# Optimization experiments

Measured on AMD Instinct MI355X. Metric: run time of the kernel, lower is better.

The kernel has to match this reference:

```python
import jax, jax.numpy as jnp
import numpy as np

B, S, D = 2, 1024, 1024
H, HD = 16, 64          # n_heads, head_dim (H*HD == D)
E, FF = 8, 2816         # num_experts, moe hidden_dim
TOP_K = 2               # hard-coded torch.topk(scores, 2)
EPS = 1e-5


def rmsnorm(x, w):
    return x * jax.lax.rsqrt(jnp.mean(x * x, axis=-1, keepdims=True) + EPS) * w


def apply_rope(x, cos, sin):
    # x: [B,S,H,HD]; cos/sin: [S,HD//2] -> interleaved rotary (llama style)
    xr, xi = x[..., 0::2], x[..., 1::2]
    c = cos[None, :, None, :]
    s = sin[None, :, None, :]
    out_r = xr * c - xi * s
    out_i = xr * s + xi * c
    return jnp.stack([out_r, out_i], axis=-1).reshape(x.shape)


def setup_inputs() -> dict:
    key = jax.random.key(0)
    ks = jax.random.split(key, 10)
    sc = 0.02
    pos = jnp.arange(S, dtype=jnp.float32)
    inv = 1.0 / (10000.0 ** (jnp.arange(0, HD, 2, dtype=jnp.float32) / HD))
    ang = pos[:, None] * inv[None, :]                       # [S, HD//2]
    return {
        "x": jax.random.normal(ks[0], (B, S, D), jnp.float32),
        "freqs_cos": jnp.cos(ang),
        "freqs_sin": jnp.sin(ang),
        "attn_norm_w": jnp.ones((D,), jnp.float32),
        "wq": jax.random.normal(ks[1], (D, D), jnp.float32) * sc,
        "wk": jax.random.normal(ks[2], (D, D), jnp.float32) * sc,
        "wv": jax.random.normal(ks[3], (D, D), jnp.float32) * sc,
        "wo": jax.random.normal(ks[4], (D, D), jnp.float32) * sc,
        "ffn_norm_w": jnp.ones((D,), jnp.float32),
        "gate_w": jax.random.normal(ks[5], (E, D), jnp.float32) * sc,
        "w1": jax.random.normal(ks[6], (E, FF, D), jnp.float32) * sc,
        "w2": jax.random.normal(ks[7], (E, FF, D), jnp.float32) * sc,
        "w3": jax.random.normal(ks[8], (E, FF, D), jnp.float32) * sc,
    }


def reference(x, freqs_cos, freqs_sin, attn_norm_w, wq, wk, wv, wo,
              ffn_norm_w, gate_w, w1, w2, w3):
    b, s, d = x.shape

    # ---- pre-norm attention + residual ----
    xn = rmsnorm(x, attn_norm_w)
    q = (xn @ wq.T).reshape(b, s, H, HD)
    k = (xn @ wk.T).reshape(b, s, H, HD)
    v = (xn @ wv.T).reshape(b, s, H, HD)
    q = apply_rope(q, freqs_cos, freqs_sin)
    k = apply_rope(k, freqs_cos, freqs_sin)
    scores = jnp.einsum("bqhd,bkhd->bhqk", q, k) / jnp.sqrt(jnp.float32(HD))
    causal = jnp.tril(jnp.ones((s, s), bool))
    scores = jnp.where(causal[None, None], scores, jnp.finfo(scores.dtype).min)
    attn = jax.nn.softmax(scores, axis=-1)
    o = jnp.einsum("bhqk,bkhd->bqhd", attn, v).reshape(b, s, d) @ wo.T
    h = x + o

    # ---- top-2 MoE FFN (math identical to gather-per-token einsums) ----
    t = rmsnorm(h, ffn_norm_w).reshape(-1, d)               # [T, D]
    T = t.shape[0]
    gate = t @ gate_w.T                                     # [T, E]
    expert_weights, expert_idx = jax.lax.top_k(gate, TOP_K)
    expert_weights = jax.nn.softmax(expert_weights, axis=-1)  # [T, 2]

    x1 = jax.nn.silu(jnp.einsum("td,efd->tef", t, w1))      # [T, E, FF]
    x3 = jnp.einsum("td,efd->tef", t, w3)                   # [T, E, FF]
    ta = jnp.arange(T)[:, None]
    g = x1[ta, expert_idx] * x3[ta, expert_idx]             # [T, 2, FF]
    gw = g * expert_weights[..., None]                      # fold routing weights
    h_full = jnp.zeros((T, E, FF), t.dtype).at[ta, expert_idx].add(gw)
    moe = jnp.einsum("tef,efd->td", h_full, w2)             # [T, D]

    return h + moe.reshape(b, s, d)
```

## Files before the change

kernel.cpp:

```cpp
#include <hip/hip_runtime.h>

#define DI __device__ __forceinline__

typedef __attribute__((ext_vector_type(8))) short short8;
typedef __attribute__((ext_vector_type(4))) float f32x4;

#define DM   1024
#define TT   2048
#define SEQ  1024
#define NHD  16
#define HDD  64
#define NE   8
#define FF   2816

DI ushort f2bf(float f){
  union { float f; unsigned u; } c; c.f = f;
  unsigned u = c.u;
  u += 0x7fffu + ((u >> 16) & 1u);
  return (ushort)(u >> 16);
}
DI float bf2f(ushort b){
  union { unsigned u; float f; } c; c.u = ((unsigned)b) << 16;
  return c.f;
}
DI unsigned pk2(float a, float b){ return (unsigned)f2bf(a) | ((unsigned)f2bf(b) << 16); }
DI uint2 mku2(unsigned a, unsigned b){ uint2 r; r.x = a; r.y = b; return r; }

DI f32x4 MFMA(short8 a, short8 b, f32x4 c){
  return __builtin_amdgcn_mfma_f32_16x16x32_bf16(a, b, c, 0, 0, 0);
}

DI void gload16(const void* g, void* l){
  __builtin_amdgcn_global_load_lds(
      (const __attribute__((address_space(1))) unsigned*)g,
      (__attribute__((address_space(3))) unsigned*)l, 16, 0, 0);
}

#define LDSWZB(row, p) (((row) * 128) + ((((p) ^ ((row) & 7))) * 16))

__global__ __launch_bounds__(256) void k_rmsnorm(const float* __restrict__ x,
                                                 const float* __restrict__ w,
                                                 ushort* __restrict__ xh,
                                                 ushort* __restrict__ xl)
{
  int row = blockIdx.x, tid = threadIdx.x;
  float4 v = ((const float4*)(x + (size_t)row * DM))[tid];
  float ss = v.x*v.x + v.y*v.y + v.z*v.z + v.w*v.w;
#pragma unroll
  for (int m = 32; m >= 1; m >>= 1) ss += __shfl_xor(ss, m);
  __shared__ float sh[4];
  if ((tid & 63) == 0) sh[tid >> 6] = ss;
  __syncthreads();
  ss = sh[0] + sh[1] + sh[2] + sh[3];
  float rstd = 1.0f / sqrtf(ss * (1.0f / DM) + 1e-5f);
  float4 wv = ((const float4*)w)[tid];
  float o0 = v.x * rstd * wv.x, o1 = v.y * rstd * wv.y;
  float o2 = v.z * rstd * wv.z, o3 = v.w * rstd * wv.w;
  ushort h0 = f2bf(o0), h1 = f2bf(o1), h2 = f2bf(o2), h3 = f2bf(o3);
  ((uint2*)(xh + (size_t)row * DM))[tid] =
      mku2((unsigned)h0 | ((unsigned)h1 << 16), (unsigned)h2 | ((unsigned)h3 << 16));
  ((uint2*)(xl + (size_t)row * DM))[tid] =
      mku2(pk2(o0 - bf2f(h0), o1 - bf2f(h1)), pk2(o2 - bf2f(h2), o3 - bf2f(h3)));
}

__global__ __launch_bounds__(256) void k_wsplit(
    const float* __restrict__ wq, const float* __restrict__ wk,
    const float* __restrict__ wv, const float* __restrict__ wo,
    ushort* __restrict__ qh, ushort* __restrict__ ql,
    ushort* __restrict__ kh, ushort* __restrict__ kl,
    ushort* __restrict__ vh, ushort* __restrict__ vl,
    ushort* __restrict__ oh, ushort* __restrict__ ol)
{
  int y = blockIdx.y;
  const float* W = y == 0 ? wq : (y == 1 ? wk : (y == 2 ? wv : wo));
  ushort* H = y == 0 ? qh : (y == 1 ? kh : (y == 2 ? vh : oh));
  ushort* L = y == 0 ? ql : (y == 1 ? kl : (y == 2 ? vl : ol));
  int i = blockIdx.x * 256 + threadIdx.x;
  float4 v = ((const float4*)W)[i];
  ushort h0 = f2bf(v.x), h1 = f2bf(v.y), h2 = f2bf(v.z), h3 = f2bf(v.w);
  ((uint2*)H)[i] = mku2((unsigned)h0 | ((unsigned)h1 << 16),
                        (unsigned)h2 | ((unsigned)h3 << 16));
  ((uint2*)L)[i] = mku2(pk2(v.x - bf2f(h0), v.y - bf2f(h1)),
                        pk2(v.z - bf2f(h2), v.w - bf2f(h3)));
}

__global__ __launch_bounds__(256) void k_cw13(const float* __restrict__ w1,
                                              const float* __restrict__ w3,
                                              ushort* __restrict__ w1b,
                                              ushort* __restrict__ w3b)
{
  const float* src = blockIdx.y ? w3 : w1;
  ushort* dst = blockIdx.y ? w3b : w1b;
  const size_t N4 = (size_t)NE * FF * DM / 4;
  for (size_t i = (size_t)blockIdx.x * 256 + threadIdx.x; i < N4;
       i += (size_t)gridDim.x * 256) {
    float4 v = ((const float4*)src)[i];
    ((uint2*)dst)[i] = mku2(pk2(v.x, v.y), pk2(v.z, v.w));
  }
}

__global__ __launch_bounds__(256) void k_tw2(const float* __restrict__ w2, ushort* __restrict__ w2t)
{
  int dt = blockIdx.x, ft = blockIdx.y, e = blockIdx.z;
  __shared__ ushort lt[64*72];
  int tid = threadIdx.x;
#pragma unroll
  for (int i = 0; i < 4; i++) {
    int c = tid + i*256;
    int r = c >> 4, q = c & 15;
    float4 v = *(const float4*)(w2 + ((size_t)e*FF + ft*64 + r) * DM + dt*64 + q*4);
    lt[(q*4+0)*72 + r] = f2bf(v.x);
    lt[(q*4+1)*72 + r] = f2bf(v.y);
    lt[(q*4+2)*72 + r] = f2bf(v.z);
    lt[(q*4+3)*72 + r] = f2bf(v.w);
  }
  __syncthreads();
#pragma unroll
  for (int i = 0; i < 2; i++) {
    int c = tid + i*256;
    int d = c >> 3, fq = c & 7;
    *(uint4*)(w2t + ((size_t)e*DM + dt*64 + d) * FF + ft*64 + fq*8) = *(const uint4*)&lt[d*72 + fq*8];
  }
}

__global__ __launch_bounds__(256, 2) void k_gemm_qkv(
    const ushort* __restrict__ xh, const ushort* __restrict__ xl,
    const ushort* __restrict__ wqh, const ushort* __restrict__ wql,
    const ushort* __restrict__ wkh, const ushort* __restrict__ wkl,
    const ushort* __restrict__ wvh, const ushort* __restrict__ wvl,
    const float* __restrict__ fc, const float* __restrict__ fs,
    ushort* __restrict__ qh, ushort* __restrict__ ql,
    ushort* __restrict__ kh, ushort* __restrict__ kl,
    ushort* __restrict__ vh, ushort* __restrict__ vl)
{
  __shared__ __align__(16) char lds[65536];
  char* Ah = lds;          char* Al = lds + 16384;
  char* Bh = lds + 32768;  char* Bl = lds + 49152;
  int bn = blockIdx.x, bm = blockIdx.y;
  int which = bn >> 3, bnn = bn & 7;
  const ushort* WH = which == 0 ? wqh : (which == 1 ? wkh : wvh);
  const ushort* WL = which == 0 ? wql : (which == 1 ? wkl : wvl);
  int tid = threadIdx.x, lane = tid & 63, w = tid >> 6, wr = w >> 1, wc = w & 1;
  int r0 = lane >> 3, pp = lane & 7;
  size_t asrc[4], bsrc[4]; int cdst[4];
#pragma unroll
  for (int i = 0; i < 4; i++) {
    int c = w * 4 + i;
    int row = c * 8 + r0;
    asrc[i] = (size_t)(bm * 128 + row) * DM + (pp ^ r0) * 8;
    bsrc[i] = (size_t)(bnn * 128 + row) * DM + (pp ^ r0) * 8;
    cdst[i] = c * 1024;
  }
  f32x4 acc[4][4] = {};
  for (int kb = 0; kb < DM; kb += 64) {
    __syncthreads();
#pragma unroll
    for (int i = 0; i < 4; i++) {
      gload16(xh + asrc[i] + kb, Ah + cdst[i]);
      gload16(xl + asrc[i] + kb, Al + cdst[i]);
      gload16(WH + bsrc[i] + kb, Bh + cdst[i]);
      gload16(WL + bsrc[i] + kb, Bl + cdst[i]);
    }
    __syncthreads();
#pragma unroll
    for (int kk = 0; kk < 2; kk++) {
      int j = kk * 4 + (lane >> 4);
      short8 ar[4], al[4];
#pragma unroll
      for (int mi = 0; mi < 4; mi++) {
        int row = wr * 64 + mi * 16 + (lane & 15);
        ar[mi] = *(const short8*)(Ah + LDSWZB(row, j));
        al[mi] = *(const short8*)(Al + LDSWZB(row, j));
      }
#pragma unroll
      for (int ni = 0; ni < 4; ni++) {
        int n = wc * 64 + ni * 16 + (lane & 15);
        short8 b_h = *(const short8*)(Bh + LDSWZB(n, j));
        short8 b_l = *(const short8*)(Bl + LDSWZB(n, j));
#pragma unroll
        for (int mi = 0; mi < 4; mi++) {
          acc[mi][ni] = MFMA(ar[mi], b_h, acc[mi][ni]);
          acc[mi][ni] = MFMA(al[mi], b_h, acc[mi][ni]);
          acc[mi][ni] = MFMA(ar[mi], b_l, acc[mi][ni]);
        }
      }
    }
  }
  ushort* OH = which == 0 ? qh : kh;
  ushort* OL = which == 0 ? ql : kl;
#pragma unroll
  for (int mi = 0; mi < 4; mi++)
#pragma unroll
    for (int ni = 0; ni < 4; ni++)
#pragma unroll
      for (int r = 0; r < 4; r++) {
        int rg = bm*128 + wr*64 + mi*16 + (lane >> 4)*4 + r;
        int cg = bnn*128 + wc*64 + ni*16 + (lane & 15);
        float v = acc[mi][ni][r];
        int b = rg >> 10, s = rg & 1023, hh = cg >> 6, hd = cg & 63;
        if (which <= 1) {
          float p = __shfl_xor(v, 1);
          int pi = hd >> 1;
          float c = fc[s*32 + pi], sn = fs[s*32 + pi];
          float rr = (hd & 1) ? (p * sn + v * c) : (v * c - p * sn);
          size_t o = ((size_t)(b*NHD + hh) * SEQ + s) * HDD + hd;
          ushort hv = f2bf(rr);
          OH[o] = hv; OL[o] = f2bf(rr - bf2f(hv));
        } else {
          size_t o = ((size_t)((b*NHD + hh)*HDD + hd)) * SEQ + s;
          ushort hv = f2bf(v);
          vh[o] = hv; vl[o] = f2bf(v - bf2f(hv));
        }
      }
}

__global__ __launch_bounds__(256) void k_attn_prep(
    const ushort* __restrict__ qh_, const ushort* __restrict__ ql_,
    const ushort* __restrict__ kh_, const ushort* __restrict__ kl_,
    const ushort* __restrict__ vh_, const ushort* __restrict__ vl_,
    ushort* __restrict__ oh_, ushort* __restrict__ ol_,
    const float* __restrict__ w1, const float* __restrict__ w3,
    ushort* __restrict__ w1b, ushort* __restrict__ w3b,
    const float* __restrict__ w2, ushort* __restrict__ w2t)
{
  __shared__ __align__(16) char smem[49152];
  int bid = blockIdx.x, tid = threadIdx.x;

  if (bid >= 1024) {
    ushort* lt = (ushort*)smem;
    int pid = bid - 1024;
    for (int tt = pid; tt < 16*44*8; tt += 512) {
      int dt = tt & 15, rest = tt >> 4;
      int ft = rest % 44, e = rest / 44;
#pragma unroll
      for (int i = 0; i < 4; i++) {
        int c = tid + i*256;
        int r = c >> 4, q = c & 15;
        float4 v = *(const float4*)(w2 + ((size_t)e*FF + ft*64 + r) * DM + dt*64 + q*4);
        lt[(q*4+0)*72 + r] = f2bf(v.x);
        lt[(q*4+1)*72 + r] = f2bf(v.y);
        lt[(q*4+2)*72 + r] = f2bf(v.z);
        lt[(q*4+3)*72 + r] = f2bf(v.w);
      }
      __syncthreads();
#pragma unroll
      for (int i = 0; i < 2; i++) {
        int c = tid + i*256;
        int d = c >> 3, fq = c & 7;
        *(uint4*)(w2t + ((size_t)e*DM + dt*64 + d) * FF + ft*64 + fq*8) =
            *(const uint4*)&lt[d*72 + fq*8];
      }
      __syncthreads();
    }
    return;
  }
  if (bid >= 512) {
    int pid = bid - 512;
    const size_t N4 = (size_t)NE * FF * DM / 4;
    for (size_t i = (size_t)pid * 256 + tid; i < N4; i += (size_t)512 * 256) {
      float4 v = ((const float4*)w1)[i];
      ((uint2*)w1b)[i] = mku2(pk2(v.x, v.y), pk2(v.z, v.w));
      float4 u = ((const float4*)w3)[i];
      ((uint2*)w3b)[i] = mku2(pk2(u.x, u.y), pk2(u.z, u.w));
    }
    return;
  }

  char* Kh = smem;          char* Kl = smem + 8192;
  char* Vh = smem + 16384;  char* Vl = smem + 24576;
  ushort* Ph = (ushort*)(smem + 32768);
  ushort* Pl = (ushort*)(smem + 40960);
  int qt = bid & 15, bh = bid >> 4;
  int lane = tid & 63, w = tid >> 6;
  int r0 = lane >> 3, pp = lane & 7;
  short8 qfh[2], qfl[2];
  int qrow = qt*64 + w*16 + (lane & 15);
#pragma unroll
  for (int ks = 0; ks < 2; ks++) {
    size_t g = ((size_t)bh * SEQ + qrow) * HDD + ks*32 + (lane >> 4)*8;
    qfh[ks] = *(const short8*)(qh_ + g);
    qfl[ks] = *(const short8*)(ql_ + g);
  }
  size_t kbase[2], vbase[2];
#pragma unroll
  for (int i = 0; i < 2; i++) {
    int c = 2*w + i;
    kbase[i] = ((size_t)bh * SEQ + c*8 + r0) * 64 + (pp ^ r0) * 8;
    vbase[i] = ((size_t)bh * 64 + c*8 + r0) * SEQ + (pp ^ r0) * 8;
  }
  f32x4 oacc[4] = {};
  float mrun[4], lrun[4];
#pragma unroll
  for (int r = 0; r < 4; r++) { mrun[r] = -1e30f; lrun[r] = 0.0f; }

  for (int kt = 0; kt <= qt; kt++) {
    __syncthreads();
#pragma unroll
    for (int i = 0; i < 2; i++) {
      int c = 2*w + i;
      size_t ko = kbase[i] + (size_t)kt * 64 * 64;
      size_t vo = vbase[i] + (size_t)kt * 64;
      gload16(kh_ + ko, Kh + c*1024);
      gload16(kl_ + ko, Kl + c*1024);
      gload16(vh_ + vo, Vh + c*1024);
      gload16(vl_ + vo, Vl + c*1024);
    }
    __syncthreads();
    f32x4 sa[4] = {};
#pragma unroll
    for (int j2 = 0; j2 < 4; j2++) {
#pragma unroll
      for (int ks = 0; ks < 2; ks++) {
        int kr = j2*16 + (lane & 15);
        int j = ks*4 + (lane >> 4);
        short8 b_h = *(const short8*)(Kh + LDSWZB(kr, j));
        short8 b_l = *(const short8*)(Kl + LDSWZB(kr, j));
        sa[j2] = MFMA(qfh[ks], b_h, sa[j2]);
        sa[j2] = MFMA(qfl[ks], b_h, sa[j2]);
        sa[j2] = MFMA(qfh[ks], b_l, sa[j2]);
      }
    }
    float sv[4][4];
#pragma unroll
    for (int j2 = 0; j2 < 4; j2++)
#pragma unroll
      for (int r = 0; r < 4; r++) {
        float xx = sa[j2][r] * 0.125f;
        if (kt == qt) {
          int kv = j2*16 + (lane & 15), qi = w*16 + (lane >> 4)*4 + r;
          if (kv > qi) xx = -1e30f;
        }
        sv[j2][r] = xx;
      }
#pragma unroll
    for (int r = 0; r < 4; r++) {
      float mx = fmaxf(fmaxf(sv[0][r], sv[1][r]), fmaxf(sv[2][r], sv[3][r]));
#pragma unroll
      for (int m = 8; m >= 1; m >>= 1) mx = fmaxf(mx, __shfl_xor(mx, m));
      float mn = fmaxf(mrun[r], mx);
      float alp = __expf(mrun[r] - mn);
      mrun[r] = mn;
      float rs = 0.0f;
#pragma unroll
      for (int j2 = 0; j2 < 4; j2++) { float pv = __expf(sv[j2][r] - mn); sv[j2][r] = pv; rs += pv; }
#pragma unroll
      for (int m = 8; m >= 1; m >>= 1) rs += __shfl_xor(rs, m);
      lrun[r] = lrun[r] * alp + rs;
#pragma unroll
      for (int hf = 0; hf < 4; hf++) oacc[hf][r] *= alp;
    }
#pragma unroll
    for (int j2 = 0; j2 < 4; j2++)
#pragma unroll
      for (int r = 0; r < 4; r++) {
        int row = (lane >> 4)*4 + r, col = j2*16 + (lane & 15);
        int d = w*1024 + row*64 + (((col >> 3) ^ (row & 7)) * 8) + (col & 7);
        ushort hv = f2bf(sv[j2][r]);
        Ph[d] = hv; Pl[d] = f2bf(sv[j2][r] - bf2f(hv));
      }
#pragma unroll
    for (int hf = 0; hf < 4; hf++) {
#pragma unroll
      for (int ks = 0; ks < 2; ks++) {
        int prow = lane & 15;
        int j = ks*4 + (lane >> 4);
        int pg = (j ^ (prow & 7)) * 8;
        short8 pfh = *(const short8*)&Ph[w*1024 + prow*64 + pg];
        short8 pfl = *(const short8*)&Pl[w*1024 + prow*64 + pg];
        int vrow = hf*16 + (lane & 15);
        short8 vfh = *(const short8*)(Vh + LDSWZB(vrow, j));
        short8 vfl = *(const short8*)(Vl + LDSWZB(vrow, j));
        oacc[hf] = MFMA(pfh, vfh, oacc[hf]);
        oacc[hf] = MFMA(pfl, vfh, oacc[hf]);
        oacc[hf] = MFMA(pfh, vfl, oacc[hf]);
      }
    }
  }
  int b = bh >> 4, h = bh & 15;
#pragma unroll
  for (int r = 0; r < 4; r++) {
    float li = 1.0f / lrun[r];
    int srow = qt*64 + w*16 + (lane >> 4)*4 + r;
#pragma unroll
    for (int hf = 0; hf < 4; hf++) {
      float v = oacc[hf][r] * li;
      size_t o = ((size_t)(b*SEQ + srow)) * DM + h*HDD + hf*16 + (lane & 15);
      ushort hv = f2bf(v);
      oh_[o] = hv; ol_[o] = f2bf(v - bf2f(hv));
    }
  }
}

__global__ __launch_bounds__(256, 3) void k_gemm_wo(
    const ushort* __restrict__ oh, const ushort* __restrict__ ol,
    const ushort* __restrict__ woh, const ushort* __restrict__ wol,
    const float* __restrict__ x, float* __restrict__ hb)
{
  __shared__ __align__(16) char lds[49152];
  char* Ah = lds;          char* Al = lds + 8192;
  char* Bh = lds + 16384;  char* Bl = lds + 32768;
  int bnn = blockIdx.x, bm = blockIdx.y;
  int tid = threadIdx.x, lane = tid & 63, w = tid >> 6;
  int r0 = lane >> 3, pp = lane & 7;
  size_t asrc[2]; int adst[2];
#pragma unroll
  for (int i = 0; i < 2; i++) {
    int c = w * 2 + i;
    int row = c * 8 + r0;
    asrc[i] = (size_t)(bm * 64 + row) * DM + (pp ^ r0) * 8;
    adst[i] = c * 1024;
  }
  size_t bsrc[4]; int bdst[4];
#pragma unroll
  for (int i = 0; i < 4; i++) {
    int c = w * 4 + i;
    int row = c * 8 + r0;
    bsrc[i] = (size_t)(bnn * 128 + row) * DM + (pp ^ r0) * 8;
    bdst[i] = c * 1024;
  }
  f32x4 acc[4][2] = {};
  for (int kb = 0; kb < DM; kb += 64) {
    __syncthreads();
#pragma unroll
    for (int i = 0; i < 2; i++) {
      gload16(oh + asrc[i] + kb, Ah + adst[i]);
      gload16(ol + asrc[i] + kb, Al + adst[i]);
    }
#pragma unroll
    for (int i = 0; i < 4; i++) {
      gload16(woh + bsrc[i] + kb, Bh + bdst[i]);
      gload16(wol + bsrc[i] + kb, Bl + bdst[i]);
    }
    __syncthreads();
#pragma unroll
    for (int kk = 0; kk < 2; kk++) {
      int j = kk * 4 + (lane >> 4);
      short8 ar[4], al[4];
#pragma unroll
      for (int mi = 0; mi < 4; mi++) {
        int row = mi * 16 + (lane & 15);
        ar[mi] = *(const short8*)(Ah + LDSWZB(row, j));
        al[mi] = *(const short8*)(Al + LDSWZB(row, j));
      }
#pragma unroll
      for (int ni = 0; ni < 2; ni++) {
        int n = w * 32 + ni * 16 + (lane & 15);
        short8 b_h = *(const short8*)(Bh + LDSWZB(n, j));
        short8 b_l = *(const short8*)(Bl + LDSWZB(n, j));
#pragma unroll
        for (int mi = 0; mi < 4; mi++) {
          acc[mi][ni] = MFMA(ar[mi], b_h, acc[mi][ni]);
          acc[mi][ni] = MFMA(al[mi], b_h, acc[mi][ni]);
          acc[mi][ni] = MFMA(ar[mi], b_l, acc[mi][ni]);
        }
      }
    }
  }
#pragma unroll
  for (int mi = 0; mi < 4; mi++)
#pragma unroll
    for (int ni = 0; ni < 2; ni++)
#pragma unroll
      for (int r = 0; r < 4; r++) {
        int rg = bm*64 + mi*16 + (lane >> 4)*4 + r;
        int cg = bnn*128 + w*32 + ni*16 + (lane & 15);
        hb[(size_t)rg * DM + cg] = x[(size_t)rg * DM + cg] + acc[mi][ni][r];
      }
}

__global__ __launch_bounds__(256) void k_gate(
    const float* __restrict__ hb, const float* __restrict__ fw, const float* __restrict__ gwt,
    ushort* __restrict__ tb, int* __restrict__ idx, float* __restrict__ ew, int* __restrict__ cnt)
{
  int t = blockIdx.x, tid = threadIdx.x;
  float4 v = ((const float4*)(hb + (size_t)t * DM))[tid];
  float ss = v.x*v.x + v.y*v.y + v.z*v.z + v.w*v.w;
#pragma unroll
  for (int m = 32; m >= 1; m >>= 1) ss += __shfl_xor(ss, m);
  __shared__ float sh[4];
  if ((tid & 63) == 0) sh[tid >> 6] = ss;
  __syncthreads();
  ss = sh[0] + sh[1] + sh[2] + sh[3];
  float rstd = 1.0f / sqrtf(ss * (1.0f / DM) + 1e-5f);
  float4 wv = ((const float4*)fw)[tid];
  float tv0 = v.x*rstd*wv.x, tv1 = v.y*rstd*wv.y, tv2 = v.z*rstd*wv.z, tv3 = v.w*rstd*wv.w;
  ((uint2*)(tb + (size_t)t * DM))[tid] = mku2(pk2(tv0, tv1), pk2(tv2, tv3));
  float ge[8];
#pragma unroll
  for (int e = 0; e < 8; e++) {
    float4 gv = ((const float4*)(gwt + (size_t)e * DM))[tid];
    float s = tv0*gv.x + tv1*gv.y + tv2*gv.z + tv3*gv.w;
#pragma unroll
    for (int m = 32; m >= 1; m >>= 1) s += __shfl_xor(s, m);
    ge[e] = s;
  }
  __shared__ float gsh[4][8];
  if ((tid & 63) == 0) {
#pragma unroll
    for (int e = 0; e < 8; e++) gsh[tid >> 6][e] = ge[e];
  }
  __syncthreads();
  if (tid == 0) {
    float lg[8];
#pragma unroll
    for (int e = 0; e < 8; e++) lg[e] = gsh[0][e] + gsh[1][e] + gsh[2][e] + gsh[3][e];
    int i0 = 0;
    for (int e = 1; e < 8; e++) if (lg[e] > lg[i0]) i0 = e;
    int i1 = (i0 == 0) ? 1 : 0;
    for (int e = 0; e < 8; e++) if (e != i0 && lg[e] > lg[i1]) i1 = e;
    float ex = __expf(lg[i1] - lg[i0]);
    idx[2*t] = i0; idx[2*t+1] = i1;
    ew[2*t] = 1.0f / (1.0f + ex); ew[2*t+1] = ex / (1.0f + ex);
    atomicAdd(&cnt[i0], 1); atomicAdd(&cnt[i1], 1);
  }
}

__global__ void k_offsets(const int* __restrict__ cnt, int* __restrict__ off,
                          int* __restrict__ fil, int* __restrict__ tmap)
{
  if (threadIdx.x == 0 && blockIdx.x == 0) {
    int a = 0, nt = 0;
    for (int e = 0; e < 8; e++) {
      off[e] = a; a += cnt[e]; fil[e] = 0;
      int m = (cnt[e] + 127) >> 7;
      for (int j = 0; j < m; j++) { tmap[1 + nt] = (e << 8) | j; nt++; }
    }
    tmap[0] = nt;
  }
}

__global__ __launch_bounds__(256) void k_scatter(
    const int* __restrict__ idx, const int* __restrict__ off,
    int* __restrict__ fil, int* __restrict__ ent, int* __restrict__ pos)
{
  int t = blockIdx.x * 256 + threadIdx.x;
  if (t < TT) {
#pragma unroll
    for (int k = 0; k < 2; k++) {
      int e = idx[2*t + k];
      int p = atomicAdd(&fil[e], 1);
      int g = off[e] + p;
      ent[g] = 2*t + k;
      pos[2*t + k] = g;
    }
  }
}

__global__ __launch_bounds__(256, 4) void k_moe13(
    const ushort* __restrict__ tb, const ushort* __restrict__ w1b, const ushort* __restrict__ w3b,
    const int* __restrict__ ent, const float* __restrict__ ew,
    const int* __restrict__ cnt, const int* __restrict__ off, const int* __restrict__ tmap,
    ushort* __restrict__ gb)
{
  int y = blockIdx.y;
  if (y >= tmap[0]) return;
  int tm = tmap[1 + y];
  int e = tm >> 8, mt = tm & 255;
  int nt = blockIdx.x;
  int cn = cnt[e], oe = off[e];
  __shared__ __align__(16) char lds[32768];
  char* Ab = lds;
  char* B1 = lds + 16384;
  char* B3 = lds + 24576;
  int tid = threadIdx.x, lane = tid & 63, w = tid >> 6;
  int wr = w >> 1, wc = w & 1;
  int r0 = lane >> 3, pp = lane & 7;

  const ushort* abase = tb + (pp ^ r0) * 8;
  unsigned aoff[4];
#pragma unroll
  for (int i = 0; i < 4; i++) {
    int c = w * 4 + i;
    int r = c * 8 + r0;
    int g = oe + mt * 128 + r; if (g > 2*TT - 1) g = 2*TT - 1;
    aoff[i] = (unsigned)((ent[g] >> 1) * DM);
  }
  size_t bofs[2];
#pragma unroll
  for (int i = 0; i < 2; i++) {
    int c = 2 * w + i;
    bofs[i] = ((size_t)e * FF + nt * 64 + c * 8 + r0) * DM + (pp ^ r0) * 8;
  }

  f32x4 acc1[4][2] = {}, acc3[4][2] = {};

  for (int kb = 0; kb < DM; kb += 64) {
    __syncthreads();
#pragma unroll
    for (int i = 0; i < 4; i++)
      gload16(abase + aoff[i] + kb, Ab + (w * 4 + i) * 1024);
#pragma unroll
    for (int i = 0; i < 2; i++) {
      gload16(w1b + bofs[i] + kb, B1 + (2 * w + i) * 1024);
      gload16(w3b + bofs[i] + kb, B3 + (2 * w + i) * 1024);
    }
    __syncthreads();
#pragma unroll
    for (int kk = 0; kk < 2; kk++) {
      int j = kk * 4 + (lane >> 4);
      short8 af[4];
#pragma unroll
      for (int mi = 0; mi < 4; mi++) {
        int row = wr * 64 + mi * 16 + (lane & 15);
        af[mi] = *(const short8*)(Ab + LDSWZB(row, j));
      }
#pragma unroll
      for (int ni = 0; ni < 2; ni++) {
        int n = wc * 32 + ni * 16 + (lane & 15);
        short8 b1f = *(const short8*)(B1 + LDSWZB(n, j));
        short8 b3f = *(const short8*)(B3 + LDSWZB(n, j));
#pragma unroll
        for (int mi = 0; mi < 4; mi++) {
          acc1[mi][ni] = MFMA(af[mi], b1f, acc1[mi][ni]);
          acc3[mi][ni] = MFMA(af[mi], b3f, acc3[mi][ni]);
        }
      }
    }
  }
#pragma unroll
  for (int mi = 0; mi < 4; mi++)
#pragma unroll
    for (int ni = 0; ni < 2; ni++)
#pragma unroll
      for (int r = 0; r < 4; r++) {
        int grow = mt * 128 + wr * 64 + mi * 16 + (lane >> 4) * 4 + r;
        if (grow < cn) {
          int g = oe + grow;
          float gwv = ew[ent[g]];
          int f = nt * 64 + wc * 32 + ni * 16 + (lane & 15);
          float x1 = acc1[mi][ni][r], x3 = acc3[mi][ni][r];
          float sg = x1 / (1.0f + __expf(-x1));
          gb[(size_t)g * FF + f] = f2bf(sg * x3 * gwv);
        }
      }
}

__global__ __launch_bounds__(256, 4) void k_moe2(
    const ushort* __restrict__ gb, const ushort* __restrict__ w2t,
    const int* __restrict__ cnt, const int* __restrict__ off, const int* __restrict__ tmap,
    float* __restrict__ mr)
{
  int y = blockIdx.y;
  if (y >= tmap[0]) return;
  int tm = tmap[1 + y];
  int e = tm >> 8, mt = tm & 255;
  int nt = blockIdx.x;
  int cn = cnt[e], oe = off[e];
  __shared__ __align__(16) char lds[24576];
  char* Ab = lds; char* Bb = lds + 16384;
  int tid = threadIdx.x, lane = tid & 63, w = tid >> 6;
  int r0 = lane >> 3, pp = lane & 7;

  const ushort* abase = gb + (pp ^ r0) * 8;
  unsigned aoff[4];
#pragma unroll
  for (int i = 0; i < 4; i++) {
    int c = w * 4 + i;
    int r = c * 8 + r0;
    int g = oe + mt * 128 + r; if (g > 2*TT - 1) g = 2*TT - 1;
    aoff[i] = (unsigned)(g * FF);
  }
  size_t bofs[2];
#pragma unroll
  for (int i = 0; i < 2; i++) {
    int c = 2 * w + i;
    bofs[i] = ((size_t)e * DM + nt * 64 + c * 8 + r0) * FF + (pp ^ r0) * 8;
  }

  f32x4 a2[2][4] = {};
  for (int kb = 0; kb < FF; kb += 64) {
    __syncthreads();
#pragma unroll
    for (int i = 0; i < 4; i++)
      gload16(abase + aoff[i] + kb, Ab + (w * 4 + i) * 1024);
#pragma unroll
    for (int i = 0; i < 2; i++)
      gload16(w2t + bofs[i] + kb, Bb + (2 * w + i) * 1024);
    __syncthreads();
#pragma unroll
    for (int kk = 0; kk < 2; kk++) {
      int j = kk * 4 + (lane >> 4);
      short8 af[2], bf[4];
#pragma unroll
      for (int mi = 0; mi < 2; mi++) {
        int row = w * 32 + mi * 16 + (lane & 15);
        af[mi] = *(const short8*)(Ab + LDSWZB(row, j));
      }
#pragma unroll
      for (int ni = 0; ni < 4; ni++) {
        int n = ni * 16 + (lane & 15);
        bf[ni] = *(const short8*)(Bb + LDSWZB(n, j));
      }
#pragma unroll
      for (int ni = 0; ni < 4; ni++)
#pragma unroll
        for (int mi = 0; mi < 2; mi++)
          a2[mi][ni] = MFMA(af[mi], bf[ni], a2[mi][ni]);
    }
  }
#pragma unroll
  for (int mi = 0; mi < 2; mi++)
#pragma unroll
    for (int ni = 0; ni < 4; ni++)
#pragma unroll
      for (int r = 0; r < 4; r++) {
        int grow = mt * 128 + w * 32 + mi * 16 + (lane >> 4) * 4 + r;
        if (grow < cn) {
          int cg = nt * 64 + ni * 16 + (lane & 15);
          mr[(size_t)(oe + grow) * DM + cg] = a2[mi][ni][r];
        }
      }
}

__global__ __launch_bounds__(256) void k_final(
    const float* __restrict__ hb, const float* __restrict__ mr,
    const int* __restrict__ pos, float* __restrict__ out)
{
  int t = blockIdx.x, tid = threadIdx.x;
  int g0 = pos[2*t], g1 = pos[2*t+1];
  float4 a  = ((const float4*)(hb + (size_t)t * DM))[tid];
  float4 m0 = ((const float4*)(mr + (size_t)g0 * DM))[tid];
  float4 m1 = ((const float4*)(mr + (size_t)g1 * DM))[tid];
  float4 o;
  o.x = a.x + m0.x + m1.x; o.y = a.y + m0.y + m1.y;
  o.z = a.z + m0.z + m1.z; o.w = a.w + m0.w + m1.w;
  ((float4*)(out + (size_t)t * DM))[tid] = o;
}

extern "C" void kernel_launch(void* const* d_in, const int* in_sizes, int n_in,
                              void* d_out, int out_size, void* d_ws, size_t ws_size,
                              hipStream_t stream)
{
  const float* x   = (const float*)d_in[0];
  const float* fc  = (const float*)d_in[1];
  const float* fs  = (const float*)d_in[2];
  const float* anw = (const float*)d_in[3];
  const float* wq  = (const float*)d_in[4];
  const float* wk  = (const float*)d_in[5];
  const float* wv  = (const float*)d_in[6];
  const float* wo  = (const float*)d_in[7];
  const float* fnw = (const float*)d_in[8];
  const float* gwm = (const float*)d_in[9];
  const float* w1  = (const float*)d_in[10];
  const float* w2  = (const float*)d_in[11];
  const float* w3  = (const float*)d_in[12];
  float* out = (float*)d_out;

  char* p = (char*)d_ws;
  auto alloc = [&](size_t n) { char* r = p; p += (n + 255) & ~(size_t)255; return r; };
  ushort* xnh = (ushort*)alloc((size_t)TT*DM*2);
  ushort* xnl = (ushort*)alloc((size_t)TT*DM*2);
  char*   pad = alloc((size_t)8*1024*1024);
  ushort* qh  = (ushort*)alloc((size_t)TT*DM*2);
  ushort* ql  = (ushort*)alloc((size_t)TT*DM*2);
  ushort* kh  = (ushort*)alloc((size_t)TT*DM*2);
  ushort* kl  = (ushort*)alloc((size_t)TT*DM*2);
  ushort* vh  = (ushort*)alloc((size_t)TT*DM*2);
  ushort* vl  = (ushort*)alloc((size_t)TT*DM*2);
  ushort* oh  = (ushort*)alloc((size_t)TT*DM*2);
  ushort* ol  = (ushort*)alloc((size_t)TT*DM*2);
  float*  hb  = (float*) alloc((size_t)TT*DM*4);
  ushort* tb  = (ushort*)alloc((size_t)TT*DM*2);
  ushort* w2t = (ushort*)alloc((size_t)NE*FF*DM*2);
  ushort* gb  = (ushort*)alloc((size_t)2*TT*FF*2);
  float*  mr  = (float*) alloc((size_t)2*TT*DM*4);
  int*    idx = (int*)   alloc((size_t)2*TT*4);
  float*  ew  = (float*) alloc((size_t)2*TT*4);
  int*    ent = (int*)   alloc((size_t)2*TT*4);
  int*    pos = (int*)   alloc((size_t)2*TT*4);
  int*    cnt = (int*)   alloc(32);
  int*    off = (int*)   alloc(32);
  int*    fil = (int*)   alloc(32);
  int*    tmap= (int*)   alloc(256);
  (void)pad;

  ushort* wsp = (ushort*)mr;
  const size_t WN = (size_t)DM * DM;
  ushort* wqh = wsp;        ushort* wql = wsp + WN;
  ushort* wkh = wsp + 2*WN; ushort* wkl = wsp + 3*WN;
  ushort* wvh = wsp + 4*WN; ushort* wvl = wsp + 5*WN;
  ushort* woh = wsp + 6*WN; ushort* wol = wsp + 7*WN;

  ushort* w3b = (ushort*)alloc((size_t)NE*FF*DM*2);
  ushort* w1b_fresh = (ushort*)alloc((size_t)NE*FF*DM*2);
  bool big = ((size_t)(p - (char*)d_ws) <= ws_size);
  ushort* w1b = big ? w1b_fresh : (ushort*)d_ws;

  hipMemsetAsync(cnt, 0, 32, stream);
  k_rmsnorm<<<TT, 256, 0, stream>>>(x, anw, xnh, xnl);
  k_wsplit<<<dim3(1024, 4), 256, 0, stream>>>(wq, wk, wv, wo,
      wqh, wql, wkh, wkl, wvh, wvl, woh, wol);
  k_gemm_qkv<<<dim3(24, 16), 256, 0, stream>>>(xnh, xnl,
      wqh, wql, wkh, wkl, wvh, wvl, fc, fs, qh, ql, kh, kl, vh, vl);
  if (big) {
    k_attn_prep<<<1536, 256, 0, stream>>>(qh, ql, kh, kl, vh, vl, oh, ol,
        w1, w3, w1b, w3b, w2, w2t);
  } else {
    k_tw2<<<dim3(16, 44, 8), 256, 0, stream>>>(w2, w2t);
    k_attn_prep<<<512, 256, 0, stream>>>(qh, ql, kh, kl, vh, vl, oh, ol,
        w1, w3, w1b, w3b, w2, w2t);
  }
  k_gemm_wo<<<dim3(8, 32), 256, 0, stream>>>(oh, ol, woh, wol, x, hb);
  k_gate<<<TT, 256, 0, stream>>>(hb, fnw, gwm, tb, idx, ew, cnt);
  k_offsets<<<1, 64, 0, stream>>>(cnt, off, fil, tmap);
  k_scatter<<<8, 256, 0, stream>>>(idx, off, fil, ent, pos);
  if (!big) {
    k_cw13<<<dim3(2048, 2), 256, 0, stream>>>(w1, w3, w1b, w3b);
  }
  k_moe13<<<dim3(44, 48), 256, 0, stream>>>(tb, w1b, w3b, ent, ew, cnt, off, tmap, gb);
  k_moe2<<<dim3(16, 48), 256, 0, stream>>>(gb, w2t, cnt, off, tmap, mr);
  k_final<<<TT, 256, 0, stream>>>(hb, mr, pos, out);
  (void)in_sizes; (void)n_in; (void)out_size;
}
```

Baseline: 418.8 us.

## Merge prep kernels and overlap w2 transpose with QKV GEMM

Fuses the rmsnorm and attention-weight split into one launch, and moves the w2 transpose/bf16 conversion from the attention-prep kernel into extra blocks of the QKV GEMM launch, so that memory-bound transpose work runs alongside the compute-bound GEMM. The gate kernel now records per-expert slot positions from its atomic counters, and a single-block kernel computes the offsets and scatters entries, replacing two launches and the second atomic pass. This cuts launch count and rebalances work across kernels. The cost is possible contention between GEMM and transpose blocks, and a serial single-block offset/scatter kernel.

Result: faster. 393.9 us (-5.9%).

```diff
diff --git a/kernel.cpp b/kernel.cpp
--- a/kernel.cpp
+++ b/kernel.cpp
@@ -38,12 +38,33 @@
 
 #define LDSWZB(row, p) (((row) * 128) + ((((p) ^ ((row) & 7))) * 16))
 
-__global__ __launch_bounds__(256) void k_rmsnorm(const float* __restrict__ x,
-                                                 const float* __restrict__ w,
-                                                 ushort* __restrict__ xh,
-                                                 ushort* __restrict__ xl)
-{
-  int row = blockIdx.x, tid = threadIdx.x;
+__global__ __launch_bounds__(256) void k_pre(
+    const float* __restrict__ x, const float* __restrict__ anw,
+    ushort* __restrict__ xh, ushort* __restrict__ xl,
+    const float* __restrict__ wq, const float* __restrict__ wk,
+    const float* __restrict__ wv, const float* __restrict__ wo,
+    ushort* __restrict__ wqh, ushort* __restrict__ wql,
+    ushort* __restrict__ wkh, ushort* __restrict__ wkl,
+    ushort* __restrict__ wvh, ushort* __restrict__ wvl,
+    ushort* __restrict__ woh, ushort* __restrict__ wol)
+{
+  int bid = blockIdx.x, tid = threadIdx.x;
+  if (bid >= 2048) {
+    int q = bid - 2048;
+    int y = q >> 10;
+    const float* W = y == 0 ? wq : (y == 1 ? wk : (y == 2 ? wv : wo));
+    ushort* H = y == 0 ? wqh : (y == 1 ? wkh : (y == 2 ? wvh : woh));
+    ushort* L = y == 0 ? wql : (y == 1 ? wkl : (y == 2 ? wvl : wol));
+    int i = (q & 1023) * 256 + tid;
+    float4 v = ((const float4*)W)[i];
+    ushort h0 = f2bf(v.x), h1 = f2bf(v.y), h2 = f2bf(v.z), h3 = f2bf(v.w);
+    ((uint2*)H)[i] = mku2((unsigned)h0 | ((unsigned)h1 << 16),
+                          (unsigned)h2 | ((unsigned)h3 << 16));
+    ((uint2*)L)[i] = mku2(pk2(v.x - bf2f(h0), v.y - bf2f(h1)),
+                          pk2(v.z - bf2f(h2), v.w - bf2f(h3)));
+    return;
+  }
+  int row = bid;
   float4 v = ((const float4*)(x + (size_t)row * DM))[tid];
   float ss = v.x*v.x + v.y*v.y + v.z*v.z + v.w*v.w;
 #pragma unroll
@@ -53,35 +74,14 @@
   __syncthreads();
   ss = sh[0] + sh[1] + sh[2] + sh[3];
   float rstd = 1.0f / sqrtf(ss * (1.0f / DM) + 1e-5f);
-  float4 wv = ((const float4*)w)[tid];
-  float o0 = v.x * rstd * wv.x, o1 = v.y * rstd * wv.y;
-  float o2 = v.z * rstd * wv.z, o3 = v.w * rstd * wv.w;
+  float4 wv2 = ((const float4*)anw)[tid];
+  float o0 = v.x * rstd * wv2.x, o1 = v.y * rstd * wv2.y;
+  float o2 = v.z * rstd * wv2.z, o3 = v.w * rstd * wv2.w;
   ushort h0 = f2bf(o0), h1 = f2bf(o1), h2 = f2bf(o2), h3 = f2bf(o3);
   ((uint2*)(xh + (size_t)row * DM))[tid] =
       mku2((unsigned)h0 | ((unsigned)h1 << 16), (unsigned)h2 | ((unsigned)h3 << 16));
   ((uint2*)(xl + (size_t)row * DM))[tid] =
       mku2(pk2(o0 - bf2f(h0), o1 - bf2f(h1)), pk2(o2 - bf2f(h2), o3 - bf2f(h3)));
-}
-
-__global__ __launch_bounds__(256) void k_wsplit(
-    const float* __restrict__ wq, const float* __restrict__ wk,
-    const float* __restrict__ wv, const float* __restrict__ wo,
-    ushort* __restrict__ qh, ushort* __restrict__ ql,
-    ushort* __restrict__ kh, ushort* __restrict__ kl,
-    ushort* __restrict__ vh, ushort* __restrict__ vl,
-    ushort* __restrict__ oh, ushort* __restrict__ ol)
-{
-  int y = blockIdx.y;
-  const float* W = y == 0 ? wq : (y == 1 ? wk : (y == 2 ? wv : wo));
-  ushort* H = y == 0 ? qh : (y == 1 ? kh : (y == 2 ? vh : oh));
-  ushort* L = y == 0 ? ql : (y == 1 ? kl : (y == 2 ? vl : ol));
-  int i = blockIdx.x * 256 + threadIdx.x;
-  float4 v = ((const float4*)W)[i];
-  ushort h0 = f2bf(v.x), h1 = f2bf(v.y), h2 = f2bf(v.z), h3 = f2bf(v.w);
-  ((uint2*)H)[i] = mku2((unsigned)h0 | ((unsigned)h1 << 16),
-                        (unsigned)h2 | ((unsigned)h3 << 16));
-  ((uint2*)L)[i] = mku2(pk2(v.x - bf2f(h0), v.y - bf2f(h1)),
-                        pk2(v.z - bf2f(h2), v.w - bf2f(h3)));
 }
 
 __global__ __launch_bounds__(256) void k_cw13(const float* __restrict__ w1,
@@ -96,30 +96,6 @@
        i += (size_t)gridDim.x * 256) {
     float4 v = ((const float4*)src)[i];
     ((uint2*)dst)[i] = mku2(pk2(v.x, v.y), pk2(v.z, v.w));
-  }
-}
-
-__global__ __launch_bounds__(256) void k_tw2(const float* __restrict__ w2, ushort* __restrict__ w2t)
-{
-  int dt = blockIdx.x, ft = blockIdx.y, e = blockIdx.z;
-  __shared__ ushort lt[64*72];
-  int tid = threadIdx.x;
-#pragma unroll
-  for (int i = 0; i < 4; i++) {
-    int c = tid + i*256;
-    int r = c >> 4, q = c & 15;
-    float4 v = *(const float4*)(w2 + ((size_t)e*FF + ft*64 + r) * DM + dt*64 + q*4);
-    lt[(q*4+0)*72 + r] = f2bf(v.x);
-    lt[(q*4+1)*72 + r] = f2bf(v.y);
-    lt[(q*4+2)*72 + r] = f2bf(v.z);
-    lt[(q*4+3)*72 + r] = f2bf(v.w);
-  }
-  __syncthreads();
-#pragma unroll
-  for (int i = 0; i < 2; i++) {
-    int c = tid + i*256;
-    int d = c >> 3, fq = c & 7;
-    *(uint4*)(w2t + ((size_t)e*DM + dt*64 + d) * FF + ft*64 + fq*8) = *(const uint4*)&lt[d*72 + fq*8];
   }
 }
 
@@ -131,16 +107,48 @@
     const float* __restrict__ fc, const float* __restrict__ fs,
     ushort* __restrict__ qh, ushort* __restrict__ ql,
     ushort* __restrict__ kh, ushort* __restrict__ kl,
-    ushort* __restrict__ vh, ushort* __restrict__ vl)
+    ushort* __restrict__ vh, ushort* __restrict__ vl,
+    const float* __restrict__ w2, ushort* __restrict__ w2t)
 {
   __shared__ __align__(16) char lds[65536];
+  int bid = blockIdx.x, tid = threadIdx.x;
+
+  if (bid >= 384) {
+    ushort* lt = (ushort*)lds;
+    int pid = bid - 384;
+    for (int tt = pid; tt < 16*44*8; tt += 512) {
+      int dt = tt & 15, rest = tt >> 4;
+      int ft = rest % 44, e = rest / 44;
+#pragma unroll
+      for (int i = 0; i < 4; i++) {
+        int c = tid + i*256;
+        int r = c >> 4, q = c & 15;
+        float4 v = *(const float4*)(w2 + ((size_t)e*FF + ft*64 + r) * DM + dt*64 + q*4);
+        lt[(q*4+0)*72 + r] = f2bf(v.x);
+        lt[(q*4+1)*72 + r] = f2bf(v.y);
+        lt[(q*4+2)*72 + r] = f2bf(v.z);
+        lt[(q*4+3)*72 + r] = f2bf(v.w);
+      }
+      __syncthreads();
+#pragma unroll
+      for (int i = 0; i < 2; i++) {
+        int c = tid + i*256;
+        int d = c >> 3, fq = c & 7;
+        *(uint4*)(w2t + ((size_t)e*DM + dt*64 + d) * FF + ft*64 + fq*8) =
+            *(const uint4*)&lt[d*72 + fq*8];
+      }
+      __syncthreads();
+    }
+    return;
+  }
+
   char* Ah = lds;          char* Al = lds + 16384;
   char* Bh = lds + 32768;  char* Bl = lds + 49152;
-  int bn = blockIdx.x, bm = blockIdx.y;
+  int bn = bid % 24, bm = bid / 24;
   int which = bn >> 3, bnn = bn & 7;
   const ushort* WH = which == 0 ? wqh : (which == 1 ? wkh : wvh);
   const ushort* WL = which == 0 ? wql : (which == 1 ? wkl : wvl);
-  int tid = threadIdx.x, lane = tid & 63, w = tid >> 6, wr = w >> 1, wc = w & 1;
+  int lane = tid & 63, w = tid >> 6, wr = w >> 1, wc = w & 1;
   int r0 = lane >> 3, pp = lane & 7;
   size_t asrc[4], bsrc[4]; int cdst[4];
 #pragma unroll
@@ -220,40 +228,11 @@
     const ushort* __restrict__ vh_, const ushort* __restrict__ vl_,
     ushort* __restrict__ oh_, ushort* __restrict__ ol_,
     const float* __restrict__ w1, const float* __restrict__ w3,
-    ushort* __restrict__ w1b, ushort* __restrict__ w3b,
-    const float* __restrict__ w2, ushort* __restrict__ w2t)
+    ushort* __restrict__ w1b, ushort* __restrict__ w3b)
 {
   __shared__ __align__(16) char smem[49152];
   int bid = blockIdx.x, tid = threadIdx.x;
 
-  if (bid >= 1024) {
-    ushort* lt = (ushort*)smem;
-    int pid = bid - 1024;
-    for (int tt = pid; tt < 16*44*8; tt += 512) {
-      int dt = tt & 15, rest = tt >> 4;
-      int ft = rest % 44, e = rest / 44;
-#pragma unroll
-      for (int i = 0; i < 4; i++) {
-        int c = tid + i*256;
-        int r = c >> 4, q = c & 15;
-        float4 v = *(const float4*)(w2 + ((size_t)e*FF + ft*64 + r) * DM + dt*64 + q*4);
-        lt[(q*4+0)*72 + r] = f2bf(v.x);
-        lt[(q*4+1)*72 + r] = f2bf(v.y);
-        lt[(q*4+2)*72 + r] = f2bf(v.z);
-        lt[(q*4+3)*72 + r] = f2bf(v.w);
-      }
-      __syncthreads();
-#pragma unroll
-      for (int i = 0; i < 2; i++) {
-        int c = tid + i*256;
-        int d = c >> 3, fq = c & 7;
-        *(uint4*)(w2t + ((size_t)e*DM + dt*64 + d) * FF + ft*64 + fq*8) =
-            *(const uint4*)&lt[d*72 + fq*8];
-      }
-      __syncthreads();
-    }
-    return;
-  }
   if (bid >= 512) {
     int pid = bid - 512;
     const size_t N4 = (size_t)NE * FF * DM / 4;
@@ -470,7 +449,8 @@
 
 __global__ __launch_bounds__(256) void k_gate(
     const float* __restrict__ hb, const float* __restrict__ fw, const float* __restrict__ gwt,
-    ushort* __restrict__ tb, int* __restrict__ idx, float* __restrict__ ew, int* __restrict__ cnt)
+    ushort* __restrict__ tb, int* __restrict__ idx, float* __restrict__ ew,
+    int* __restrict__ cnt, int* __restrict__ pos)
 {
   int t = blockIdx.x, tid = threadIdx.x;
   float4 v = ((const float4*)(hb + (size_t)t * DM))[tid];
@@ -511,38 +491,32 @@
     float ex = __expf(lg[i1] - lg[i0]);
     idx[2*t] = i0; idx[2*t+1] = i1;
     ew[2*t] = 1.0f / (1.0f + ex); ew[2*t+1] = ex / (1.0f + ex);
-    atomicAdd(&cnt[i0], 1); atomicAdd(&cnt[i1], 1);
-  }
-}
-
-__global__ void k_offsets(const int* __restrict__ cnt, int* __restrict__ off,
-                          int* __restrict__ fil, int* __restrict__ tmap)
-{
-  if (threadIdx.x == 0 && blockIdx.x == 0) {
+    pos[2*t]   = atomicAdd(&cnt[i0], 1);
+    pos[2*t+1] = atomicAdd(&cnt[i1], 1);
+  }
+}
+
+__global__ __launch_bounds__(256) void k_offscatter(
+    const int* __restrict__ cnt, int* __restrict__ off, int* __restrict__ tmap,
+    const int* __restrict__ idx, int* __restrict__ ent, int* __restrict__ pos)
+{
+  __shared__ int soff[8];
+  int tid = threadIdx.x;
+  if (tid == 0) {
     int a = 0, nt = 0;
     for (int e = 0; e < 8; e++) {
-      off[e] = a; a += cnt[e]; fil[e] = 0;
+      off[e] = a; soff[e] = a; a += cnt[e];
       int m = (cnt[e] + 127) >> 7;
       for (int j = 0; j < m; j++) { tmap[1 + nt] = (e << 8) | j; nt++; }
     }
     tmap[0] = nt;
   }
-}
-
-__global__ __launch_bounds__(256) void k_scatter(
-    const int* __restrict__ idx, const int* __restrict__ off,
-    int* __restrict__ fil, int* __restrict__ ent, int* __restrict__ pos)
-{
-  int t = blockIdx.x * 256 + threadIdx.x;
-  if (t < TT) {
-#pragma unroll
-    for (int k = 0; k < 2; k++) {
-      int e = idx[2*t + k];
-      int p = atomicAdd(&fil[e], 1);
-      int g = off[e] + p;
-      ent[g] = 2*t + k;
-      pos[2*t + k] = g;
-    }
+  __syncthreads();
+  for (int s = tid; s < 2*TT; s += 256) {
+    int e = idx[s];
+    int g = soff[e] + pos[s];
+    ent[g] = s;
+    pos[s] = g;
   }
 }
 
@@ -770,7 +744,6 @@
   int*    pos = (int*)   alloc((size_t)2*TT*4);
   int*    cnt = (int*)   alloc(32);
   int*    off = (int*)   alloc(32);
-  int*    fil = (int*)   alloc(32);
   int*    tmap= (int*)   alloc(256);
   (void)pad;
 
@@ -787,23 +760,20 @@
   ushort* w1b = big ? w1b_fresh : (ushort*)d_ws;
 
   hipMemsetAsync(cnt, 0, 32, stream);
-  k_rmsnorm<<<TT, 256, 0, stream>>>(x, anw, xnh, xnl);
-  k_wsplit<<<dim3(1024, 4), 256, 0, stream>>>(wq, wk, wv, wo,
+  k_pre<<<6144, 256, 0, stream>>>(x, anw, xnh, xnl, wq, wk, wv, wo,
       wqh, wql, wkh, wkl, wvh, wvl, woh, wol);
-  k_gemm_qkv<<<dim3(24, 16), 256, 0, stream>>>(xnh, xnl,
-      wqh, wql, wkh, wkl, wvh, wvl, fc, fs, qh, ql, kh, kl, vh, vl);
+  k_gemm_qkv<<<896, 256, 0, stream>>>(xnh, xnl,
+      wqh, wql, wkh, wkl, wvh, wvl, fc, fs, qh, ql, kh, kl, vh, vl, w2, w2t);
   if (big) {
-    k_attn_prep<<<1536, 256, 0, stream>>>(qh, ql, kh, kl, vh, vl, oh, ol,
-        w1, w3, w1b, w3b, w2, w2t);
+    k_attn_prep<<<1024, 256, 0, stream>>>(qh, ql, kh, kl, vh, vl, oh, ol,
+        w1, w3, w1b, w3b);
   } else {
-    k_tw2<<<dim3(16, 44, 8), 256, 0, stream>>>(w2, w2t);
     k_attn_prep<<<512, 256, 0, stream>>>(qh, ql, kh, kl, vh, vl, oh, ol,
-        w1, w3, w1b, w3b, w2, w2t);
+        w1, w3, w1b, w3b);
   }
   k_gemm_wo<<<dim3(8, 32), 256, 0, stream>>>(oh, ol, woh, wol, x, hb);
-  k_gate<<<TT, 256, 0, stream>>>(hb, fnw, gwm, tb, idx, ew, cnt);
-  k_offsets<<<1, 64, 0, stream>>>(cnt, off, fil, tmap);
-  k_scatter<<<8, 256, 0, stream>>>(idx, off, fil, ent, pos);
+  k_gate<<<TT, 256, 0, stream>>>(hb, fnw, gwm, tb, idx, ew, cnt, pos);
+  k_offscatter<<<1, 256, 0, stream>>>(cnt, off, tmap, idx, ent, pos);
   if (!big) {
     k_cw13<<<dim3(2048, 2), 256, 0, stream>>>(w1, w3, w1b, w3b);
   }
```
